# Performance work log

Hardware: AMD Instinct MI355X
Metric: run time of the kernel (lower is better)

## Reference

```python
import jax, jax.numpy as jnp
import numpy as np

VOCAB, EMB, HID = 50000, 256, 512
N, T = 256, 512


def setup_inputs() -> dict:
    key = jax.random.key(0)
    ks = jax.random.split(key, 9)
    s_ih = 1.0 / np.sqrt(HID)
    return {
        "input1": jax.random.randint(ks[0], (N, T), 0, VOCAB, dtype=jnp.int32),
        "input2": jax.random.randint(ks[1], (N, T), 0, VOCAB, dtype=jnp.int32),
        "emb_table": jax.random.normal(ks[2], (VOCAB, EMB), jnp.float32),
        "W_ih": jax.random.normal(ks[3], (4 * HID, EMB), jnp.float32) * s_ih,
        "W_hh": jax.random.normal(ks[4], (4 * HID, HID), jnp.float32) * s_ih,
        "b_ih": jax.random.normal(ks[5], (4 * HID,), jnp.float32) * s_ih,
        "b_hh": jax.random.normal(ks[6], (4 * HID,), jnp.float32) * s_ih,
        "W_fc": jax.random.normal(ks[7], (2, HID), jnp.float32) * s_ih,
        "b_fc": jax.random.normal(ks[8], (2,), jnp.float32) * s_ih,
    }


def _lstm_last_h(tokens, emb_table, W_ih, W_hh, b):
    # tokens: [N, T] int -> embedded [N, T, E]
    x = emb_table[tokens]
    # precompute input projections for all timesteps: [T, N, 4H]
    xg = jnp.einsum("nte,ge->tng", x, W_ih) + b
    h0 = jnp.zeros((tokens.shape[0], HID), x.dtype)
    c0 = jnp.zeros_like(h0)

    def step(carry, xg_t):
        h, c = carry
        gates = xg_t + h @ W_hh.T  # [N, 4H]
        i, f, g, o = jnp.split(gates, 4, axis=-1)
        i, f, o = jax.nn.sigmoid(i), jax.nn.sigmoid(f), jax.nn.sigmoid(o)
        g = jnp.tanh(g)
        c = f * c + i * g
        h = o * jnp.tanh(c)
        return (h, c), None

    (h, _), _ = jax.lax.scan(step, (h0, c0), xg)
    return h  # [N, HID]


def reference(input1, input2, emb_table, W_ih, W_hh, b_ih, b_hh, W_fc, b_fc):
    b = b_ih + b_hh
    h1 = _lstm_last_h(input1, emb_table, W_ih, W_hh, b)
    h2 = _lstm_last_h(input2, emb_table, W_ih, W_hh, b)
    h = h1 * h2  # combo_unit == 'MULT'
    logits = h @ W_fc.T + b_fc  # [N, 2]
    return jax.nn.softmax(logits, axis=1)
```

## Files before the change

### kernel.cpp

```cpp
#include <hip/hip_runtime.h>
#include <stdint.h>

#define VOCAB  50000
#define EMBD   256
#define HIDD   512
#define G4     2048
#define NBAT   256
#define TSEQ   512

#define O_P2    0ull
#define O_EMBT  204800000ull
#define O_WIH   230400000ull
#define O_WHH   231448576ull
#define O_TOKT  233545728ull
#define O_HBUF  234594304ull
#define O_BAR   235642880ull
#define WS_NEED 235643136ull
#define O_FLAGS O_EMBT

typedef __bf16 bf16x8 __attribute__((ext_vector_type(8)));
typedef float  f32x4  __attribute__((ext_vector_type(4)));
typedef float  f32x16 __attribute__((ext_vector_type(16)));

__device__ __forceinline__ unsigned short f2bf(float x) {
  unsigned u = __float_as_uint(x);
  u = (u + 0x7fffu + ((u >> 16) & 1u)) >> 16;
  return (unsigned short)u;
}
__device__ __forceinline__ float b2f(unsigned short b) {
  return __uint_as_float(((unsigned)b) << 16);
}
__device__ __forceinline__ float sigf(float x) {
  float e = __builtin_amdgcn_exp2f(-1.4426950408889634f * x);
  return __builtin_amdgcn_rcpf(1.0f + e);
}
__device__ __forceinline__ float tanhf_(float x) {
  float e = __builtin_amdgcn_exp2f(-2.8853900817779268f * x);
  return 2.0f * __builtin_amdgcn_rcpf(1.0f + e) - 1.0f;
}

__global__ void k_prep(const float* __restrict__ emb, const float* __restrict__ wih,
                       const float* __restrict__ whh, const int* __restrict__ tok1,
                       const int* __restrict__ tok2, unsigned short* __restrict__ embT,
                       unsigned short* __restrict__ wihb, unsigned short* __restrict__ whhb,
                       int* __restrict__ tokT, unsigned* __restrict__ hz)
{
  const int stride = gridDim.x * blockDim.x;
  const int id0 = blockIdx.x * blockDim.x + threadIdx.x;
  for (int i = id0; i < VOCAB * EMBD; i += stride) embT[i] = f2bf(emb[i]);
  for (int i = id0; i < G4 * EMBD; i += stride)    wihb[i] = f2bf(wih[i]);
  for (int i = id0; i < G4 * HIDD; i += stride)    whhb[i] = f2bf(whh[i]);
  for (int i = id0; i < 2 * TSEQ * NBAT; i += stride) {
    int l = i >> 17, t = (i >> 8) & 511, n = i & 255;
    tokT[i] = (l ? tok2 : tok1)[n * TSEQ + t];
  }
  for (int i = id0; i < 262144; i += stride) hz[i] = 0u;
}

__global__ void k_zero(unsigned* __restrict__ flags)
{
  const int i = blockIdx.x * blockDim.x + threadIdx.x;
  if (i < 16384) flags[i] = 0u;
}

__global__ __launch_bounds__(256) void
k_proj(const unsigned short* __restrict__ embT, const unsigned short* __restrict__ wihb,
       const float* __restrict__ bih, const float* __restrict__ bhh,
       unsigned short* __restrict__ P2)
{
  const int l  = threadIdx.x & 63;
  const int w  = threadIdx.x >> 6;
  const int n0 = blockIdx.x * 128 + (w & 1) * 64;
  const int m0 = blockIdx.y * 128 + (w >> 1) * 64;
  const int lq = l >> 4, lc = l & 15;

  f32x4 acc[4][4];
  #pragma unroll
  for (int a = 0; a < 4; ++a)
    #pragma unroll
    for (int b = 0; b < 4; ++b) acc[a][b] = (f32x4){0.f, 0.f, 0.f, 0.f};

  const uint8_t* eb = (const uint8_t*)embT;
  const uint8_t* wb = (const uint8_t*)wihb;
  #pragma unroll
  for (int ks = 0; ks < 8; ++ks) {
    const int koff = ks * 64 + lq * 16;
    bf16x8 a[4], b[4];
    #pragma unroll
    for (int mt = 0; mt < 4; ++mt) {
      int row = m0 + mt * 16 + lc; if (row >= VOCAB) row = VOCAB - 1;
      a[mt] = *(const bf16x8*)(eb + (size_t)row * 512 + koff);
    }
    #pragma unroll
    for (int nt = 0; nt < 4; ++nt) {
      int g = n0 + nt * 16 + lc;
      b[nt] = *(const bf16x8*)(wb + (size_t)g * 512 + koff);
    }
    #pragma unroll
    for (int mt = 0; mt < 4; ++mt)
      #pragma unroll
      for (int nt = 0; nt < 4; ++nt)
        acc[mt][nt] = __builtin_amdgcn_mfma_f32_16x16x32_bf16(a[mt], b[nt], acc[mt][nt], 0, 0, 0);
  }

  #pragma unroll
  for (int mt = 0; mt < 4; ++mt)
    #pragma unroll
    for (int r = 0; r < 4; ++r) {
      const int vrow = m0 + mt * 16 + lq * 4 + r;
      if (vrow < VOCAB) {
        #pragma unroll
        for (int nt = 0; nt < 4; ++nt) {
          const int gcol = n0 + nt * 16 + lc;
          float v = acc[mt][nt][r] + bih[gcol] + bhh[gcol];
          const int colp = ((gcol & 511) << 2) | (gcol >> 9);
          P2[(size_t)vrow * 2048 + colp] = f2bf(v);
        }
      }
    }
}

#define HL 131072

__global__ __launch_bounds__(256, 1) void
k_lstm(const uint8_t* __restrict__ P2, const int* __restrict__ tokT,
       const uint8_t* __restrict__ whh, uint8_t* __restrict__ hbuf,
       unsigned* __restrict__ flags)
{
  __shared__ __align__(16) uint8_t smem[163840];
  const int tid  = threadIdx.x;
  const int l    = tid & 63;
  const int w    = tid >> 6;
  const int bid  = blockIdx.x;
  const int jb   = bid & 15;
  const int mg   = (bid >> 4) & 7;
  const int lstm = bid >> 7;
  const int grp  = bid >> 4;
  const int m0   = mg * 32;
  const int j0   = jb * 32;

  for (int i = 0; i < 32; ++i) {
    const int G = i * 256 + tid;
    const int R = G >> 6, c = G & 63;
    const uint8_t* src = whh + (size_t)((R >> 5) * 512 + j0 + (R & 31)) * 1024 + (size_t)c * 16;
    const uint4 v = *(const uint4*)src;
    *(uint4*)(smem + (size_t)R * 1024 + ((c ^ (R & 7)) * 16)) = v;
  }

  const size_t hslot = (size_t)NBAT * HIDD * 2;
  const int em   = tid >> 3;
  const int ecol = tid & 7;
  const int an   = l & 31;
  const int ah   = l >> 5;
  const int Rrow = w * 32 + an;

  const unsigned* fpoll = flags + (size_t)(grp * 16 + (l & 15)) * 64;
  unsigned* fmine = flags + (size_t)bid * 64;

  float cst[4] = {0.f, 0.f, 0.f, 0.f};
  int tok_next = tokT[(lstm * TSEQ + 0) * NBAT + m0 + em];

  for (int t = 0; t < TSEQ; ++t) {
    const int tok_cur = tok_next;

    const uint8_t* xsrc = P2 + (size_t)tok_cur * 4096 + (size_t)j0 * 8 + (size_t)ecol * 32;
    const uint4 xq0 = *(const uint4*)(xsrc);
    const uint4 xq1 = *(const uint4*)(xsrc + 16);
    if (t + 1 < TSEQ) tok_next = tokT[(lstm * TSEQ + (t + 1)) * NBAT + m0 + em];

    if (t > 0 && w == 0) {
      const unsigned tgt = (unsigned)t;
      int guard = 0;
      for (;;) {
        const unsigned v = __hip_atomic_load(fpoll, __ATOMIC_RELAXED, __HIP_MEMORY_SCOPE_AGENT);
        if (__all((int)(v >= tgt))) break;
        __builtin_amdgcn_s_sleep(1);
        if (++guard > 400000) break;
      }
    }
    __syncthreads();

    {
      const uint8_t* hb = hbuf + (size_t)(lstm * 2 + (t & 1)) * hslot
                        + (size_t)m0 * 1024 + (size_t)tid * 8;
      unsigned long long v[16];
      #pragma unroll
      for (int i = 0; i < 16; ++i)
        v[i] = __hip_atomic_load((const unsigned long long*)(hb + (size_t)i * 2048),
                                 __ATOMIC_RELAXED, __HIP_MEMORY_SCOPE_AGENT);
      #pragma unroll
      for (int i = 0; i < 16; ++i) {
        const int m = i * 2 + (tid >> 7);
        const int c = (tid >> 1) & 63;
        const int half = tid & 1;
        *(unsigned long long*)(smem + HL + (size_t)m * 1024
                               + ((c ^ (m & 7)) * 16) + half * 8) = v[i];
      }
    }
    __syncthreads();

    f32x16 acc0{}, acc1{};
    #pragma unroll 8
    for (int ks = 0; ks < 32; ++ks) {
      const int ch = ks * 2 + ah;
      const bf16x8 av = *(const bf16x8*)(smem + HL + (size_t)an * 1024 + ((ch ^ (an & 7)) * 16));
      const bf16x8 bv = *(const bf16x8*)(smem + (size_t)Rrow * 1024 + ((ch ^ (an & 7)) * 16));
      if (ks & 1) acc1 = __builtin_amdgcn_mfma_f32_32x32x16_bf16(av, bv, acc1, 0, 0, 0);
      else        acc0 = __builtin_amdgcn_mfma_f32_32x32x16_bf16(av, bv, acc0, 0, 0, 0);
    }
    __syncthreads();

    {
      float* gb = (float*)(smem + HL);
      #pragma unroll
      for (int r = 0; r < 16; ++r) {
        const int row = (r & 3) + 8 * (r >> 2) + 4 * ah;
        gb[w * 1024 + row * 32 + an] = acc0[r] + acc1[r];
      }
    }
    __syncthreads();

    {
      const float* gb = (const float*)(smem + HL);
      const f32x4 pi = *(const f32x4*)(gb + 0 * 1024 + em * 32 + ecol * 4);
      const f32x4 pf = *(const f32x4*)(gb + 1 * 1024 + em * 32 + ecol * 4);
      const f32x4 pg = *(const f32x4*)(gb + 2 * 1024 + em * 32 + ecol * 4);
      const f32x4 po = *(const f32x4*)(gb + 3 * 1024 + em * 32 + ecol * 4);
      unsigned short xsv[16];
      *(uint4*)(xsv) = xq0;
      *(uint4*)(xsv + 8) = xq1;
      unsigned short hv[4];
      #pragma unroll
      for (int k = 0; k < 4; ++k) {
        const float iv = sigf(pi[k] + b2f(xsv[k * 4 + 0]));
        const float fv = sigf(pf[k] + b2f(xsv[k * 4 + 1]));
        const float gv = tanhf_(pg[k] + b2f(xsv[k * 4 + 2]));
        const float ov = sigf(po[k] + b2f(xsv[k * 4 + 3]));
        const float cv = fv * cst[k] + iv * gv;
        cst[k] = cv;
        hv[k] = f2bf(ov * tanhf_(cv));
      }
      unsigned long long hp =
          (unsigned long long)hv[0] | ((unsigned long long)hv[1] << 16) |
          ((unsigned long long)hv[2] << 32) | ((unsigned long long)hv[3] << 48);
      uint8_t* hdst = hbuf + (size_t)(lstm * 2 + ((t + 1) & 1)) * hslot
                    + (size_t)(m0 + em) * 1024 + (size_t)(j0 + ecol * 4) * 2;
      __hip_atomic_store((unsigned long long*)hdst, hp,
                         __ATOMIC_RELAXED, __HIP_MEMORY_SCOPE_AGENT);
    }
    __syncthreads();

    if (tid == 0 && t + 1 < TSEQ)
      __hip_atomic_store(fmine, (unsigned)(t + 1),
                         __ATOMIC_RELAXED, __HIP_MEMORY_SCOPE_AGENT);
  }
}

__global__ __launch_bounds__(64) void
k_fc(const uint8_t* __restrict__ hbuf, const float* __restrict__ wfc,
     const float* __restrict__ bfc, float* __restrict__ out)
{
  const int n = blockIdx.x, l = threadIdx.x;
  const unsigned short* h1 = (const unsigned short*)(hbuf) + (size_t)n * HIDD;
  const unsigned short* h2 = (const unsigned short*)(hbuf + 2 * (size_t)NBAT * HIDD * 2) + (size_t)n * HIDD;
  float s0 = 0.f, s1 = 0.f;
  for (int j = l; j < HIDD; j += 64) {
    float hv = b2f(h1[j]) * b2f(h2[j]);
    s0 += hv * wfc[j];
    s1 += hv * wfc[HIDD + j];
  }
  #pragma unroll
  for (int off = 32; off > 0; off >>= 1) {
    s0 += __shfl_down(s0, off, 64);
    s1 += __shfl_down(s1, off, 64);
  }
  if (l == 0) {
    s0 += bfc[0]; s1 += bfc[1];
    float m  = fmaxf(s0, s1);
    float e0 = __builtin_amdgcn_exp2f((s0 - m) * 1.4426950408889634f);
    float e1 = __builtin_amdgcn_exp2f((s1 - m) * 1.4426950408889634f);
    float inv = 1.0f / (e0 + e1);
    out[n * 2 + 0] = e0 * inv;
    out[n * 2 + 1] = e1 * inv;
  }
}

extern "C" void kernel_launch(void* const* d_in, const int* in_sizes, int n_in,
                              void* d_out, int out_size, void* d_ws, size_t ws_size,
                              hipStream_t stream) {
  (void)in_sizes; (void)n_in; (void)out_size;
  if (ws_size < WS_NEED) return;

  const int*   tok1 = (const int*)d_in[0];
  const int*   tok2 = (const int*)d_in[1];
  const float* emb  = (const float*)d_in[2];
  const float* wih  = (const float*)d_in[3];
  const float* whh  = (const float*)d_in[4];
  const float* bih  = (const float*)d_in[5];
  const float* bhh  = (const float*)d_in[6];
  const float* wfc  = (const float*)d_in[7];
  const float* bfc  = (const float*)d_in[8];
  float* out = (float*)d_out;

  uint8_t* ws = (uint8_t*)d_ws;
  unsigned short* P2    = (unsigned short*)(ws + O_P2);
  unsigned short* embT  = (unsigned short*)(ws + O_EMBT);
  unsigned short* wihb  = (unsigned short*)(ws + O_WIH);
  unsigned short* whhb  = (unsigned short*)(ws + O_WHH);
  int*            tokT  = (int*)(ws + O_TOKT);
  uint8_t*        hbuf  = ws + O_HBUF;
  unsigned*       flags = (unsigned*)(ws + O_FLAGS);

  k_prep<<<1024, 256, 0, stream>>>(emb, wih, whh, tok1, tok2, embT, wihb, whhb,
                                   tokT, (unsigned*)hbuf);
  k_proj<<<dim3(16, 391), 256, 0, stream>>>(embT, wihb, bih, bhh, P2);
  k_zero<<<64, 256, 0, stream>>>(flags);

  {
    const uint8_t* p2p = (const uint8_t*)P2;
    const int*     tkp = tokT;
    const uint8_t* whp = (const uint8_t*)whhb;
    uint8_t*       hbp = hbuf;
    unsigned*      flp = flags;
    void* args[5] = {(void*)&p2p, (void*)&tkp, (void*)&whp, (void*)&hbp, (void*)&flp};
    hipError_t e = hipLaunchCooperativeKernel((void*)k_lstm, dim3(256), dim3(256),
                                              args, 0, stream);
    if (e != hipSuccess) {
      (void)hipGetLastError();
      k_lstm<<<256, 256, 0, stream>>>(p2p, tkp, whp, hbp, flp);
    }
  }

  k_fc<<<256, 64, 0, stream>>>(hbuf, wfc, bfc, out);
}
```

Baseline: 2.249 ms.

## Split LSTM batch tile into two half-phases to overlap sync with compute

The recurrent kernel now processes each block's 32 batch rows as two 16-row halves in alternating phases. Each half has its own flag and its own shared h buffer, so one half's recurrent matmul and gate math can run while the other half's producers are still finishing. The matmul moves from 32x32x16 to 16x16x32 MFMA with a new swizzled shared layout, and the gate work is split two columns per thread. This adds twice as many flag waits and barriers per step, and more flag memory to zero.

```diff
diff --git a/kernel.cpp b/kernel.cpp
--- a/kernel.cpp
+++ b/kernel.cpp
@@ -14,13 +14,13 @@
 #define O_WHH   231448576ull
 #define O_TOKT  233545728ull
 #define O_HBUF  234594304ull
-#define O_BAR   235642880ull
 #define WS_NEED 235643136ull
 #define O_FLAGS O_EMBT
 
-typedef __bf16 bf16x8 __attribute__((ext_vector_type(8)));
-typedef float  f32x4  __attribute__((ext_vector_type(4)));
-typedef float  f32x16 __attribute__((ext_vector_type(16)));
+typedef __bf16 bf16x8  __attribute__((ext_vector_type(8)));
+typedef __bf16 bf16x16 __attribute__((ext_vector_type(16)));
+typedef float  f32x4   __attribute__((ext_vector_type(4)));
+typedef unsigned long long ullx2 __attribute__((ext_vector_type(2)));
 
 __device__ __forceinline__ unsigned short f2bf(float x) {
   unsigned u = __float_as_uint(x);
@@ -60,7 +60,7 @@
 __global__ void k_zero(unsigned* __restrict__ flags)
 {
   const int i = blockIdx.x * blockDim.x + threadIdx.x;
-  if (i < 16384) flags[i] = 0u;
+  if (i < 65536) flags[i] = 0u;
 }
 
 __global__ __launch_bounds__(256) void
@@ -120,6 +120,28 @@
     }
 }
 
+__device__ __forceinline__ void stage_h16(uint8_t* dst, const uint8_t* src_base, int tid)
+{
+  const int row = tid >> 4, rem = tid & 15, q = rem >> 2, g4 = rem & 3;
+  const uint8_t* s0 = src_base + (size_t)row * 1024 + q * 16;
+  unsigned long long v[8];
+  #pragma unroll
+  for (int j = 0; j < 4; ++j) {
+    const int ks = g4 * 4 + j;
+    v[2*j]   = __hip_atomic_load((const unsigned long long*)(s0 + ks * 64),
+                                 __ATOMIC_RELAXED, __HIP_MEMORY_SCOPE_AGENT);
+    v[2*j+1] = __hip_atomic_load((const unsigned long long*)(s0 + ks * 64 + 8),
+                                 __ATOMIC_RELAXED, __HIP_MEMORY_SCOPE_AGENT);
+  }
+  uint8_t* d0 = dst + (size_t)row * 1024 + q * 256;
+  #pragma unroll
+  for (int j = 0; j < 4; ++j) {
+    const int ks = g4 * 4 + j;
+    ullx2 p; p.x = v[2*j]; p.y = v[2*j+1];
+    *(ullx2*)(d0 + (((ks >> 1) ^ (row & 7)) * 32) + (ks & 1) * 16) = p;
+  }
+}
+
 #define HL 131072
 
 __global__ __launch_bounds__(256, 1) void
@@ -142,117 +164,124 @@
   for (int i = 0; i < 32; ++i) {
     const int G = i * 256 + tid;
     const int R = G >> 6, c = G & 63;
+    const int ks = c >> 2, q = c & 3;
     const uint8_t* src = whh + (size_t)((R >> 5) * 512 + j0 + (R & 31)) * 1024 + (size_t)c * 16;
     const uint4 v = *(const uint4*)src;
-    *(uint4*)(smem + (size_t)R * 1024 + ((c ^ (R & 7)) * 16)) = v;
+    *(uint4*)(smem + (size_t)R * 1024 + q * 256 + (((ks >> 1) ^ (R & 7)) * 32) + (ks & 1) * 16) = v;
   }
 
   const size_t hslot = (size_t)NBAT * HIDD * 2;
-  const int em   = tid >> 3;
-  const int ecol = tid & 7;
-  const int an   = l & 31;
-  const int ah   = l >> 5;
-  const int Rrow = w * 32 + an;
-
-  const unsigned* fpoll = flags + (size_t)(grp * 16 + (l & 15)) * 64;
-  unsigned* fmine = flags + (size_t)bid * 64;
-
-  float cst[4] = {0.f, 0.f, 0.f, 0.f};
-  int tok_next = tokT[(lstm * TSEQ + 0) * NBAT + m0 + em];
-
-  for (int t = 0; t < TSEQ; ++t) {
-    const int tok_cur = tok_next;
-
-    const uint8_t* xsrc = P2 + (size_t)tok_cur * 4096 + (size_t)j0 * 8 + (size_t)ecol * 32;
-    const uint4 xq0 = *(const uint4*)(xsrc);
-    const uint4 xq1 = *(const uint4*)(xsrc + 16);
-    if (t + 1 < TSEQ) tok_next = tokT[(lstm * TSEQ + (t + 1)) * NBAT + m0 + em];
-
-    if (t > 0 && w == 0) {
-      const unsigned tgt = (unsigned)t;
-      int guard = 0;
-      for (;;) {
-        const unsigned v = __hip_atomic_load(fpoll, __ATOMIC_RELAXED, __HIP_MEMORY_SCOPE_AGENT);
-        if (__all((int)(v >= tgt))) break;
-        __builtin_amdgcn_s_sleep(1);
-        if (++guard > 400000) break;
+  const int arow = l & 15;
+  const int q4   = l >> 4;
+  const int erow = tid >> 4;
+  const int ecg  = tid & 15;
+
+  float cA0 = 0.f, cA1 = 0.f, cB0 = 0.f, cB1 = 0.f;
+  uint4 xqA, xqB;
+
+  {
+    const int tok = tokT[(lstm * TSEQ + 0) * NBAT + m0 + erow];
+    xqA = *(const uint4*)(P2 + (size_t)tok * 4096 + (size_t)(j0 + ecg * 2) * 8);
+    stage_h16(smem + HL, hbuf + (size_t)(lstm * 2) * hslot + (size_t)m0 * 1024, tid);
+  }
+
+  for (int ph = 0; ph < 2 * TSEQ; ++ph) {
+    const int s = ph & 1, t = ph >> 1;
+    uint8_t* hb = smem + HL + s * 16384;
+
+    __syncthreads();
+
+    f32x4 acc0 = {0.f,0.f,0.f,0.f}, acc1 = {0.f,0.f,0.f,0.f};
+    {
+      const uint8_t* abase  = hb + (size_t)arow * 1024 + q4 * 256;
+      const uint8_t* b0base = smem + (size_t)(w * 32 + arow) * 1024 + q4 * 256;
+      const uint8_t* b1base = b0base + 16 * 1024;
+      const int sw = arow & 7;
+      #pragma unroll
+      for (int ksp = 0; ksp < 8; ++ksp) {
+        const int off = (ksp ^ sw) * 32;
+        const bf16x16 av = *(const bf16x16*)(abase + off);
+        const bf16x16 b0 = *(const bf16x16*)(b0base + off);
+        const bf16x16 b1 = *(const bf16x16*)(b1base + off);
+        const bf16x8 al = __builtin_shufflevector(av, av, 0,1,2,3,4,5,6,7);
+        const bf16x8 ah = __builtin_shufflevector(av, av, 8,9,10,11,12,13,14,15);
+        const bf16x8 b0l = __builtin_shufflevector(b0, b0, 0,1,2,3,4,5,6,7);
+        const bf16x8 b0h = __builtin_shufflevector(b0, b0, 8,9,10,11,12,13,14,15);
+        const bf16x8 b1l = __builtin_shufflevector(b1, b1, 0,1,2,3,4,5,6,7);
+        const bf16x8 b1h = __builtin_shufflevector(b1, b1, 8,9,10,11,12,13,14,15);
+        acc0 = __builtin_amdgcn_mfma_f32_16x16x32_bf16(al, b0l, acc0, 0, 0, 0);
+        acc1 = __builtin_amdgcn_mfma_f32_16x16x32_bf16(al, b1l, acc1, 0, 0, 0);
+        acc0 = __builtin_amdgcn_mfma_f32_16x16x32_bf16(ah, b0h, acc0, 0, 0, 0);
+        acc1 = __builtin_amdgcn_mfma_f32_16x16x32_bf16(ah, b1h, acc1, 0, 0, 0);
       }
     }
     __syncthreads();
 
     {
-      const uint8_t* hb = hbuf + (size_t)(lstm * 2 + (t & 1)) * hslot
-                        + (size_t)m0 * 1024 + (size_t)tid * 8;
-      unsigned long long v[16];
+      float* gb = (float*)hb;
       #pragma unroll
-      for (int i = 0; i < 16; ++i)
-        v[i] = __hip_atomic_load((const unsigned long long*)(hb + (size_t)i * 2048),
-                                 __ATOMIC_RELAXED, __HIP_MEMORY_SCOPE_AGENT);
-      #pragma unroll
-      for (int i = 0; i < 16; ++i) {
-        const int m = i * 2 + (tid >> 7);
-        const int c = (tid >> 1) & 63;
-        const int half = tid & 1;
-        *(unsigned long long*)(smem + HL + (size_t)m * 1024
-                               + ((c ^ (m & 7)) * 16) + half * 8) = v[i];
+      for (int r = 0; r < 4; ++r) {
+        gb[((q4 * 4 + r) * 32 + arow) * 4 + w]      = acc0[r];
+        gb[((q4 * 4 + r) * 32 + 16 + arow) * 4 + w] = acc1[r];
       }
     }
     __syncthreads();
 
-    f32x16 acc0{}, acc1{};
-    #pragma unroll 8
-    for (int ks = 0; ks < 32; ++ks) {
-      const int ch = ks * 2 + ah;
-      const bf16x8 av = *(const bf16x8*)(smem + HL + (size_t)an * 1024 + ((ch ^ (an & 7)) * 16));
-      const bf16x8 bv = *(const bf16x8*)(smem + (size_t)Rrow * 1024 + ((ch ^ (an & 7)) * 16));
-      if (ks & 1) acc1 = __builtin_amdgcn_mfma_f32_32x32x16_bf16(av, bv, acc1, 0, 0, 0);
-      else        acc0 = __builtin_amdgcn_mfma_f32_32x32x16_bf16(av, bv, acc0, 0, 0, 0);
+    {
+      const float* gb = (const float*)hb;
+      const int go = (erow * 32 + ecg * 2) * 4;
+      const f32x4 p0 = *(const f32x4*)(gb + go);
+      const f32x4 p1 = *(const f32x4*)(gb + go + 4);
+      unsigned short xv[8];
+      const uint4 xqs = s ? xqB : xqA;
+      *(uint4*)xv = xqs;
+      float c0 = s ? cB0 : cA0;
+      float c1 = s ? cB1 : cA1;
+      const float i0 = sigf(p0[0] + b2f(xv[0]));
+      const float f0 = sigf(p0[1] + b2f(xv[1]));
+      const float g0 = tanhf_(p0[2] + b2f(xv[2]));
+      const float o0 = sigf(p0[3] + b2f(xv[3]));
+      c0 = f0 * c0 + i0 * g0;
+      const float h0 = o0 * tanhf_(c0);
+      const float i1 = sigf(p1[0] + b2f(xv[4]));
+      const float f1 = sigf(p1[1] + b2f(xv[5]));
+      const float g1 = tanhf_(p1[2] + b2f(xv[6]));
+      const float o1 = sigf(p1[3] + b2f(xv[7]));
+      c1 = f1 * c1 + i1 * g1;
+      const float h1 = o1 * tanhf_(c1);
+      if (s) { cB0 = c0; cB1 = c1; } else { cA0 = c0; cA1 = c1; }
+      const unsigned hp = (unsigned)f2bf(h0) | ((unsigned)f2bf(h1) << 16);
+      uint8_t* hdst = hbuf + (size_t)(lstm * 2 + ((t + 1) & 1)) * hslot
+                    + (size_t)(m0 + s * 16 + erow) * 1024 + (size_t)(j0 + ecg * 2) * 2;
+      __hip_atomic_store((unsigned*)hdst, hp, __ATOMIC_RELAXED, __HIP_MEMORY_SCOPE_AGENT);
     }
     __syncthreads();
 
-    {
-      float* gb = (float*)(smem + HL);
-      #pragma unroll
-      for (int r = 0; r < 16; ++r) {
-        const int row = (r & 3) + 8 * (r >> 2) + 4 * ah;
-        gb[w * 1024 + row * 32 + an] = acc0[r] + acc1[r];
+    if (tid == 0 && t < TSEQ - 1)
+      __hip_atomic_store(flags + (size_t)(bid * 2 + s) * 64, (unsigned)(t + 1),
+                         __ATOMIC_RELAXED, __HIP_MEMORY_SCOPE_AGENT);
+
+    if (ph < 2 * TSEQ - 1) {
+      const int ns = s ^ 1;
+      const int tn = t + s;
+      const int tok = tokT[(lstm * TSEQ + tn) * NBAT + m0 + ns * 16 + erow];
+      const uint4 nx = *(const uint4*)(P2 + (size_t)tok * 4096 + (size_t)(j0 + ecg * 2) * 8);
+      if (ns) xqB = nx; else xqA = nx;
+      {
+        const unsigned tgt = (unsigned)tn;
+        const unsigned* fp = flags + (size_t)(((grp << 4) + (l & 15)) * 2 + ns) * 64;
+        int guard = 0;
+        for (;;) {
+          const unsigned v = __hip_atomic_load(fp, __ATOMIC_RELAXED, __HIP_MEMORY_SCOPE_AGENT);
+          if (__all((int)(v >= tgt))) break;
+          __builtin_amdgcn_s_sleep(1);
+          if (++guard > 400000) break;
+        }
       }
-    }
-    __syncthreads();
-
-    {
-      const float* gb = (const float*)(smem + HL);
-      const f32x4 pi = *(const f32x4*)(gb + 0 * 1024 + em * 32 + ecol * 4);
-      const f32x4 pf = *(const f32x4*)(gb + 1 * 1024 + em * 32 + ecol * 4);
-      const f32x4 pg = *(const f32x4*)(gb + 2 * 1024 + em * 32 + ecol * 4);
-      const f32x4 po = *(const f32x4*)(gb + 3 * 1024 + em * 32 + ecol * 4);
-      unsigned short xsv[16];
-      *(uint4*)(xsv) = xq0;
-      *(uint4*)(xsv + 8) = xq1;
-      unsigned short hv[4];
-      #pragma unroll
-      for (int k = 0; k < 4; ++k) {
-        const float iv = sigf(pi[k] + b2f(xsv[k * 4 + 0]));
-        const float fv = sigf(pf[k] + b2f(xsv[k * 4 + 1]));
-        const float gv = tanhf_(pg[k] + b2f(xsv[k * 4 + 2]));
-        const float ov = sigf(po[k] + b2f(xsv[k * 4 + 3]));
-        const float cv = fv * cst[k] + iv * gv;
-        cst[k] = cv;
-        hv[k] = f2bf(ov * tanhf_(cv));
-      }
-      unsigned long long hp =
-          (unsigned long long)hv[0] | ((unsigned long long)hv[1] << 16) |
-          ((unsigned long long)hv[2] << 32) | ((unsigned long long)hv[3] << 48);
-      uint8_t* hdst = hbuf + (size_t)(lstm * 2 + ((t + 1) & 1)) * hslot
-                    + (size_t)(m0 + em) * 1024 + (size_t)(j0 + ecol * 4) * 2;
-      __hip_atomic_store((unsigned long long*)hdst, hp,
-                         __ATOMIC_RELAXED, __HIP_MEMORY_SCOPE_AGENT);
-    }
-    __syncthreads();
-
-    if (tid == 0 && t + 1 < TSEQ)
-      __hip_atomic_store(fmine, (unsigned)(t + 1),
-                         __ATOMIC_RELAXED, __HIP_MEMORY_SCOPE_AGENT);
+      stage_h16(smem + HL + ns * 16384,
+                hbuf + (size_t)(lstm * 2 + (tn & 1)) * hslot + (size_t)(m0 + ns * 16) * 1024,
+                tid);
+    }
   }
 }
 
@@ -314,7 +343,7 @@
   k_prep<<<1024, 256, 0, stream>>>(emb, wih, whh, tok1, tok2, embT, wihb, whhb,
                                    tokT, (unsigned*)hbuf);
   k_proj<<<dim3(16, 391), 256, 0, stream>>>(embT, wihb, bih, bhh, P2);
-  k_zero<<<64, 256, 0, stream>>>(flags);
+  k_zero<<<256, 256, 0, stream>>>(flags);
 
   {
     const uint8_t* p2p = (const uint8_t*)P2;
```

Measured after the change: 3.682 ms. 63.7% more time.
